# Optimization experiments

Hardware: AMD Instinct MI355X
Metric: run time of the kernel (lower is better)

Reference implementation:

```python
import jax, jax.numpy as jnp
import numpy as np

N = 100000   # nodes
E = 1600000  # edges
IN = 3       # in_channels
H = 32       # hidden_channels
C = 10       # num_classes_dynamic (== num output classes here)
G = 64       # number of graphs in the batch


def setup_inputs() -> dict:
    key = jax.random.key(0)
    ks = jax.random.split(key, 12)
    def w(k, shape, fan_in):
        return jax.random.normal(k, shape, jnp.float32) / np.sqrt(fan_in).astype(np.float32)
    inp = {}
    inp["x"] = jax.random.normal(ks[0], (N, IN), jnp.float32)
    inp["edge_index"] = jax.random.randint(ks[1], (2, E), 0, N, jnp.int32)
    inp["batch"] = jnp.sort(jax.random.randint(ks[2], (N,), 0, G, jnp.int32))
    # per-class linear filters (DynamicEdgeConv.filters)
    inp["filt_W"] = w(ks[3], (C, IN, H), IN)
    inp["filt_b"] = jnp.zeros((C, H), jnp.float32)
    # shared edge MLP: Linear(2H,H) -> ReLU -> Linear(H,H)
    inp["mlp_W1"] = w(ks[4], (2 * H, H), 2 * H)
    inp["mlp_b1"] = jnp.zeros((H,), jnp.float32)
    inp["mlp_W2"] = w(ks[5], (H, H), H)
    inp["mlp_b2"] = jnp.zeros((H,), jnp.float32)
    # GCN layers (gcn1 input dim hardcoded 323 = IN + C*H)
    inp["gcn1_W"] = w(ks[6], (IN + C * H, H), IN + C * H)
    inp["gcn1_b"] = jnp.zeros((H,), jnp.float32)
    inp["gcn2_W"] = w(ks[7], (H, H), H)
    inp["gcn2_b"] = jnp.zeros((H,), jnp.float32)
    # classifier
    inp["cls_W"] = w(ks[8], (H, C), H)
    inp["cls_b"] = jnp.zeros((C,), jnp.float32)
    return inp


def _gcn_conv(x, W, b, row, col, dinv):
    # PyG GCNConv: add self-loops, sym-normalize, aggregate src->dst
    xw = x @ W                                   # [N, H]
    norm = dinv[row] * dinv[col]                 # [E]
    out = jax.ops.segment_sum(xw[row] * norm[:, None], col, num_segments=x.shape[0])
    out = out + xw * (dinv * dinv)[:, None]      # self-loop term, norm = 1/deg_i
    return out + b


def _forward(x, edge_index, batch, filt_W, filt_b, mlp_W1, mlp_b1, mlp_W2, mlp_b2,
             gcn1_W, gcn1_b, gcn2_W, gcn2_b, cls_W, cls_b):
    row, col = edge_index[0], edge_index[1]
    n = x.shape[0]

    # DynamicEdgeConv: per-class filter -> gather(row,col) -> edge MLP -> scatter_add into col
    def per_class(_, wb):
        Wc, bc = wb
        xc = x @ Wc + bc                                      # [N, H]
        ef = jnp.concatenate([xc[row], xc[col]], axis=1)      # [E, 2H]
        h = jax.nn.relu(ef @ mlp_W1 + mlp_b1) @ mlp_W2 + mlp_b2
        return None, jax.ops.segment_sum(h, col, num_segments=n)
    _, aggs = jax.lax.scan(per_class, None, (filt_W, filt_b))  # [C, N, H]

    feat = jnp.concatenate([x, aggs.transpose(1, 0, 2).reshape(n, -1)], axis=1)  # [N, IN + C*H]

    deg = jax.ops.segment_sum(jnp.ones(row.shape[0], x.dtype), col, num_segments=n) + 1.0
    dinv = deg ** -0.5
    h1 = jax.nn.relu(_gcn_conv(feat, gcn1_W, gcn1_b, row, col, dinv))
    h2 = jax.nn.relu(_gcn_conv(h1, gcn2_W, gcn2_b, row, col, dinv))

    counts = jax.ops.segment_sum(jnp.ones(n, x.dtype), batch, num_segments=G)
    pooled = jax.ops.segment_sum(h2, batch, num_segments=G) / jnp.maximum(counts, 1.0)[:, None]
    return pooled @ cls_W + cls_b                             # [G, C]


def reference(x, edge_index, batch, filt_W, filt_b, mlp_W1, mlp_b1, mlp_W2, mlp_b2,
              gcn1_W, gcn1_b, gcn2_W, gcn2_b, cls_W, cls_b):
    return _forward(x, edge_index, batch, filt_W, filt_b, mlp_W1, mlp_b1, mlp_W2, mlp_b2,
                    gcn1_W, gcn1_b, gcn2_W, gcn2_b, cls_W, cls_b)
```

## Files before the change

kernel.cpp:

```cpp
#include <hip/hip_runtime.h>

#define NN 100000
#define NE 1600000
#define HH 32
#define CC 10
#define GG 64
#define NB 391
#define PBLK 100
#define ECH 16000
#define MTOT (NB * PBLK)
#define MSB ((MTOT + 255) / 256)

typedef _Float16 half8 __attribute__((ext_vector_type(8)));
typedef _Float16 half2v __attribute__((ext_vector_type(2)));
typedef float f32x4 __attribute__((ext_vector_type(4)));

__device__ __forceinline__ half2v bch(int v) { return __builtin_bit_cast(half2v, v); }

__global__ void zero_f(float* p, int n) {
    int i = blockIdx.x * 256 + threadIdx.x;
    if (i < n) p[i] = 0.0f;
}

__global__ void precompute_small(const float* __restrict__ fW, const float* __restrict__ fb,
                                 const float* __restrict__ W1, const float* __restrict__ b1,
                                 const float* __restrict__ W2, const float* __restrict__ b2,
                                 const float* __restrict__ g1W, float* __restrict__ tab) {
    int c = blockIdx.x;
    int k = threadIdx.x >> 5;
    int j = threadIdx.x & 31;
    float m = 0.f;
    for (int mm = 0; mm < 32; ++mm)
        m += W2[k * 32 + mm] * g1W[(3 + 32 * c + mm) * 32 + j];
    tab[2240 + c * 1024 + k * 32 + j] = m;

    if (k < 3) {
        float a = 0.f, b = 0.f;
        for (int i = 0; i < 32; ++i) {
            float w = fW[c * 96 + k * 32 + i];
            a += w * W1[i * 32 + j];
            b += w * W1[(32 + i) * 32 + j];
        }
        tab[c * 96 + k * 32 + j] = a;
        tab[960 + c * 96 + k * 32 + j] = b;
    } else if (k == 3) {
        float h = b1[j];
        for (int i = 0; i < 32; ++i)
            h += fb[c * 32 + i] * (W1[i * 32 + j] + W1[(32 + i) * 32 + j]);
        tab[1920 + c * 32 + j] = h;
    } else if (k == 4 && c == 0) {
        float t = 0.f;
        for (int cc2 = 0; cc2 < CC; ++cc2)
            for (int mm = 0; mm < 32; ++mm)
                t += b2[mm] * g1W[(3 + 32 * cc2 + mm) * 32 + j];
        tab[12480 + j] = t;
    }
}

__global__ void mfrag_kernel(const float* __restrict__ tab, _Float16* __restrict__ Mfrag) {
    int gid = blockIdx.x * 256 + threadIdx.x;
    if (gid >= 1280) return;
    int set = gid >> 6, l = gid & 63;
    int kc = set >> 1, jt = set & 1;
    int j = jt * 16 + (l & 15);
    int kbase = kc * 32 + (l >> 4) * 8;
#pragma unroll
    for (int i = 0; i < 8; ++i)
        Mfrag[gid * 8 + i] = (_Float16)tab[2240 + (kbase + i) * 32 + j];
}

__global__ void bucket_hist(const int* __restrict__ ei, int* __restrict__ mat) {
    __shared__ int h[NB];
    int blk = blockIdx.x, tid = threadIdx.x;
    for (int i = tid; i < NB; i += 256) h[i] = 0;
    __syncthreads();
    int base = blk * ECH;
    for (int k = tid; k < ECH; k += 256)
        atomicAdd(&h[ei[NE + base + k] >> 8], 1);
    __syncthreads();
    for (int i = tid; i < NB; i += 256) mat[i * PBLK + blk] = h[i];
}

__global__ void scan_m1(const int* __restrict__ mat, int* __restrict__ msum) {
    __shared__ int sh[256];
    int b = blockIdx.x, t = threadIdx.x;
    int i = b * 256 + t;
    sh[t] = (i < MTOT) ? mat[i] : 0;
    __syncthreads();
    for (int off = 128; off > 0; off >>= 1) {
        if (t < off) sh[t] += sh[t + off];
        __syncthreads();
    }
    if (t == 0) msum[b] = sh[0];
}

__global__ void scan_m2(int* __restrict__ msum) {
    __shared__ int sh[256];
    int t = threadIdx.x;
    int v = (t < MSB) ? msum[t] : 0;
    sh[t] = v;
    __syncthreads();
    for (int off = 1; off < 256; off <<= 1) {
        int add = (t >= off) ? sh[t - off] : 0;
        __syncthreads();
        sh[t] += add;
        __syncthreads();
    }
    if (t < MSB) msum[t] = sh[t] - v;
}

__global__ void scan_m3(int* __restrict__ mat, const int* __restrict__ msum) {
    __shared__ int sh[256];
    int b = blockIdx.x, t = threadIdx.x;
    int i = b * 256 + t;
    int v = (i < MTOT) ? mat[i] : 0;
    sh[t] = v;
    __syncthreads();
    for (int off = 1; off < 256; off <<= 1) {
        int add = (t >= off) ? sh[t - off] : 0;
        __syncthreads();
        sh[t] += add;
        __syncthreads();
    }
    if (i < MTOT) mat[i] = sh[t] - v + msum[b];
}

__global__ void bucket_scatter(const int* __restrict__ ei, const int* __restrict__ mat,
                               unsigned int* __restrict__ part) {
    __shared__ int bas[NB];
    __shared__ int cur[NB];
    int blk = blockIdx.x, tid = threadIdx.x;
    for (int i = tid; i < NB; i += 256) { bas[i] = mat[i * PBLK + blk]; cur[i] = 0; }
    __syncthreads();
    int base = blk * ECH;
    for (int k = tid; k < ECH; k += 256) {
        int e = base + k;
        int r = ei[e];
        int c = ei[NE + e];
        int b = c >> 8;
        int local = atomicAdd(&cur[b], 1);
        part[bas[b] + local] = (unsigned)r | ((unsigned)(c & 255) << 24);
    }
}

__global__ void bucket_build(const unsigned int* __restrict__ part, const int* __restrict__ mat,
                             const float* __restrict__ x, int* __restrict__ csr_row,
                             int* __restrict__ ideg, int* __restrict__ offs,
                             float* __restrict__ dinv, float4* __restrict__ xpad,
                             uint4* __restrict__ xs) {
    __shared__ int lh[256];
    __shared__ int lex[256];
    __shared__ int cur[256];
    int b = blockIdx.x, tid = threadIdx.x;
    int ebase = mat[b * PBLK];
    int eend = (b == NB - 1) ? NE : mat[(b + 1) * PBLK];
    int m = eend - ebase;
    lh[tid] = 0;
    __syncthreads();
    for (int k = tid; k < m; k += 256) {
        unsigned v = part[ebase + k];
        atomicAdd(&lh[v >> 24], 1);
    }
    __syncthreads();
    int cnt = lh[tid];
    lex[tid] = cnt;
    __syncthreads();
    for (int off = 1; off < 256; off <<= 1) {
        int v = (tid >= off) ? lex[tid - off] : 0;
        __syncthreads();
        lex[tid] += v;
        __syncthreads();
    }
    int excl = lex[tid] - cnt;
    lex[tid] = excl;
    cur[tid] = 0;
    int n = b * 256 + tid;
    if (n < NN) {
        ideg[n] = cnt;
        offs[n] = ebase + excl;
        float di = rsqrtf((float)cnt + 1.0f);
        dinv[n] = di;
        float x0 = x[n * 3], x1 = x[n * 3 + 1], x2 = x[n * 3 + 2];
        xpad[n] = make_float4(x0, x1, x2, di);
        _Float16 hx = (_Float16)x0, hy = (_Float16)x1, hz = (_Float16)x2;
        half2v sx = {hx, hx}, sy = {hy, hy}, sz = {hz, hz};
        xs[n] = make_uint4(__builtin_bit_cast(unsigned int, sx),
                           __builtin_bit_cast(unsigned int, sy),
                           __builtin_bit_cast(unsigned int, sz), 0u);
    }
    if (b == 0 && tid == 0) offs[NN] = NE;
    __syncthreads();
    for (int k = tid; k < m; k += 256) {
        unsigned v = part[ebase + k];
        int cl = (int)(v >> 24);
        int r = (int)(v & 0x00FFFFFFu);
        int local = atomicAdd(&cur[cl], 1);
        csr_row[ebase + lex[cl] + local] = r;
    }
}

#define EC_PAIR(QQ, SRC) do { \
    half2v px_ = bch(__shfl((int)(QQ).x, (SRC), 64)); \
    half2v py_ = bch(__shfl((int)(QQ).y, (SRC), 64)); \
    half2v pz_ = bch(__shfl((int)(QQ).z, (SRC), 64)); \
    _Pragma("unroll") \
    for (int p = 0; p < 5; ++p) { \
        half2v v = va[p] + px_ * A0[p] + py_ * A1[p] + pz_ * A2[p]; \
        v = __builtin_elementwise_max(v, zero); \
        acc[p] += v; \
    } } while (0)

#define EC_FLUSH() do { \
    _Pragma("unroll") \
    for (int p = 0; p < 5; ++p) { \
        accf[2 * p]     += (float)acc[p].x; \
        accf[2 * p + 1] += (float)acc[p].y; \
        acc[p] = zero; \
    } } while (0)

#define EC_CHUNK_FROM(T0, QQ, C2) do { \
    int tfull_ = (C2) >> 1; \
    int t_ = (T0); \
    for (; t_ + 4 <= tfull_; t_ += 4) { \
        _Pragma("unroll") \
        for (int u = 0; u < 4; ++u) EC_PAIR(QQ, 2 * (t_ + u) + half); \
        EC_FLUSH(); \
    } \
    for (; t_ < tfull_; ++t_) EC_PAIR(QQ, 2 * t_ + half); \
    if ((C2) & 1) { \
        int src_ = (C2) - 1; \
        half2v px_ = bch(__shfl((int)(QQ).x, src_, 64)); \
        half2v py_ = bch(__shfl((int)(QQ).y, src_, 64)); \
        half2v pz_ = bch(__shfl((int)(QQ).z, src_, 64)); \
        if (half == 0) { \
            _Pragma("unroll") \
            for (int p = 0; p < 5; ++p) { \
                half2v v = va[p] + px_ * A0[p] + py_ * A1[p] + pz_ * A2[p]; \
                v = __builtin_elementwise_max(v, zero); \
                acc[p] += v; \
            } \
        } \
    } \
    EC_FLUSH(); } while (0)

__global__ __launch_bounds__(256, 4) void edgeconv_fused(
    const uint4* __restrict__ xs, const int* __restrict__ offs,
    const int* __restrict__ csr_row, const float* __restrict__ tab,
    _Float16* __restrict__ aggh) {
    int lane = threadIdx.x & 63;
    int j = lane & 31;
    int half = lane >> 5;

    half2v A0[5], A1[5], A2[5], B0[5], B1[5], B2[5], hb[5];
#pragma unroll
    for (int p = 0; p < 5; ++p) {
        int c0 = 2 * p, c1 = 2 * p + 1;
        A0[p] = half2v{(_Float16)tab[c0 * 96 + j],        (_Float16)tab[c1 * 96 + j]};
        A1[p] = half2v{(_Float16)tab[c0 * 96 + 32 + j],   (_Float16)tab[c1 * 96 + 32 + j]};
        A2[p] = half2v{(_Float16)tab[c0 * 96 + 64 + j],   (_Float16)tab[c1 * 96 + 64 + j]};
        B0[p] = half2v{(_Float16)tab[960 + c0 * 96 + j],      (_Float16)tab[960 + c1 * 96 + j]};
        B1[p] = half2v{(_Float16)tab[960 + c0 * 96 + 32 + j], (_Float16)tab[960 + c1 * 96 + 32 + j]};
        B2[p] = half2v{(_Float16)tab[960 + c0 * 96 + 64 + j], (_Float16)tab[960 + c1 * 96 + 64 + j]};
        hb[p] = half2v{(_Float16)tab[1920 + c0 * 32 + j], (_Float16)tab[1920 + c1 * 32 + j]};
    }
    const half2v zero = half2v{(_Float16)0.f, (_Float16)0.f};

    int wid = blockIdx.x * 4 + (threadIdx.x >> 6);
    const int ws = gridDim.x * 4;

    int n = wid;
    if (n >= NN) return;
    int e0 = offs[n];
    int e1 = offs[n + 1];
    uint4 qn = xs[n];
    int n2 = n + ws;
    int e0n = 0, e1n = 0;
    if (n2 < NN) { e0n = offs[n2]; e1n = offs[n2 + 1]; }
    uint4 q;
    {
        int ee = e0 + lane;
        int r0 = (ee < e1) ? csr_row[ee] : 0;
        q = xs[r0];
    }

    while (true) {
        int n3 = n2 + ws;
        int e0n2 = 0, e1n2 = 0;
        if (n3 < NN) { e0n2 = offs[n3]; e1n2 = offs[n3 + 1]; }
        uint4 qn2 = make_uint4(0u, 0u, 0u, 0u);
        if (n2 < NN) qn2 = xs[n2];

        bool multi = (e1 - e0) > 64;
        int pb = multi ? (e0 + 64) : e0n;
        int pe = multi ? e1 : e1n;
        int ee2 = pb + lane;
        int rn = (ee2 < pe) ? csr_row[ee2] : 0;

        half2v pxn = bch((int)qn.x), pyn = bch((int)qn.y), pzn = bch((int)qn.z);
        half2v va[5], acc[5];
        float accf[10];
#pragma unroll
        for (int p = 0; p < 5; ++p) {
            va[p] = hb[p] + pxn * B0[p] + pyn * B1[p] + pzn * B2[p];
            acc[p] = zero;
            accf[2 * p] = 0.f;
            accf[2 * p + 1] = 0.f;
        }

        int c2 = e1 - e0;
        if (c2 > 64) c2 = 64;
        int t0 = 0;
        if ((c2 >> 1) >= 4) {
#pragma unroll
            for (int u = 0; u < 4; ++u) EC_PAIR(q, 2 * u + half);
            EC_FLUSH();
            t0 = 4;
        }
        uint4 qpre = xs[rn];
        EC_CHUNK_FROM(t0, q, c2);

        if (multi) {
            int base = e0 + 64;
            uint4 qc = qpre;
            while (true) {
                int cc = e1 - base;
                if (cc > 64) cc = 64;
                int nb = base + 64;
                bool m2 = nb < e1;
                int pb2 = m2 ? nb : e0n;
                int pe2 = m2 ? e1 : e1n;
                int ee3 = pb2 + lane;
                int rn2 = (ee3 < pe2) ? csr_row[ee3] : 0;
                uint4 qp2 = xs[rn2];
                EC_CHUNK_FROM(0, qc, cc);
                qc = qp2;
                if (!m2) break;
                base = nb;
            }
            qpre = qc;
        }

#pragma unroll
        for (int c = 0; c < 10; ++c) accf[c] += __shfl_xor(accf[c], 32, 64);
        _Float16* arow = aggh + (size_t)n * 320 + j;
#pragma unroll
        for (int i = 0; i < 5; ++i) {
            int c = half * 5 + i;
            __builtin_nontemporal_store((_Float16)accf[c], arow + c * 32);
        }

        if (n2 >= NN) return;
        n = n2;
        n2 = n3;
        e0 = e0n; e1 = e1n;
        e0n = e0n2; e1n = e1n2;
        qn = qn2;
        q = qpre;
    }
}

__global__ __launch_bounds__(256) void fold_mfma(
    const _Float16* __restrict__ aggh, const _Float16* __restrict__ MfragG,
    const float4* __restrict__ xpad, const int* __restrict__ ideg,
    const float* __restrict__ tab, const float* __restrict__ g1W,
    _Float16* __restrict__ y1) {
    __shared__ _Float16 Mf[10240];
    {
        const uint4* src = (const uint4*)MfragG;
        uint4* dst = (uint4*)Mf;
        for (int i = threadIdx.x; i < 1280; i += 256) dst[i] = src[i];
    }
    __syncthreads();

    int wave = blockIdx.x * 4 + (threadIdx.x >> 6);
    int lane = threadIdx.x & 63;
    int n0 = wave * 16;
    if (n0 >= NN) return;

    int m = lane & 15, q = lane >> 4;
    int arow_n = n0 + m;
    bool rowok = arow_n < NN;
    const _Float16* arow = aggh + (size_t)arow_n * 320 + q * 8;

    const half8* mf = (const half8*)Mf;
    f32x4 acc0 = {0.f, 0.f, 0.f, 0.f};
    f32x4 acc1 = {0.f, 0.f, 0.f, 0.f};

    for (int kc = 0; kc < 10; ++kc) {
        half8 a;
        if (rowok) a = *(const half8*)(arow + kc * 32);
        else {
#pragma unroll
            for (int i = 0; i < 8; ++i) a[i] = (_Float16)0.f;
        }
        half8 b0 = mf[(kc * 2 + 0) * 64 + lane];
        half8 b1 = mf[(kc * 2 + 1) * 64 + lane];
        acc0 = __builtin_amdgcn_mfma_f32_16x16x32_f16(a, b0, acc0, 0, 0, 0);
        acc1 = __builtin_amdgcn_mfma_f32_16x16x32_f16(a, b1, acc1, 0, 0, 0);
    }

    int jcol = lane & 15;
    float t0 = tab[12480 + jcol],      t1 = tab[12480 + 16 + jcol];
    float w00 = g1W[jcol],      w01 = g1W[32 + jcol],      w02 = g1W[64 + jcol];
    float w10 = g1W[16 + jcol], w11 = g1W[48 + jcol],      w12 = g1W[80 + jcol];
#pragma unroll
    for (int r = 0; r < 4; ++r) {
        int node = n0 + q * 4 + r;
        if (node < NN) {
            float4 xn = xpad[node];
            float dg = (float)ideg[node];
            float v0 = dg * t0 + xn.x * w00 + xn.y * w01 + xn.z * w02 + acc0[r];
            float v1 = dg * t1 + xn.x * w10 + xn.y * w11 + xn.z * w12 + acc1[r];
            y1[node * 32 + jcol]      = (_Float16)(v0 * xn.w);
            y1[node * 32 + 16 + jcol] = (_Float16)(v1 * xn.w);
        }
    }
}

__global__ __launch_bounds__(256, 8) void prop1_fused(
    const int* __restrict__ offs, const int* __restrict__ csr_row,
    const unsigned int* __restrict__ y1p, const float* __restrict__ dinv,
    const float* __restrict__ g1b, const float* __restrict__ g2W,
    unsigned int* __restrict__ y2p) {
    __shared__ float g2s[1024];
    for (int i = threadIdx.x; i < 1024; i += 256) g2s[i] = g2W[i];
    __syncthreads();

    int lane = threadIdx.x & 63;
    int l = lane & 15;
    int wid = blockIdx.x * 4 + (threadIdx.x >> 6);
    int n = wid * 4 + (lane >> 4);
    if (n >= NN) return;

    int e0 = offs[n], e1 = offs[n + 1];
    float sAl = 0.f, sAh = 0.f, sBl = 0.f, sBh = 0.f;
    int e = e0;
    if (e + 7 < e1) {
        int r[8];
#pragma unroll
        for (int u = 0; u < 8; ++u) r[u] = csr_row[e + u];
        while (true) {
            half2v p[8];
#pragma unroll
            for (int u = 0; u < 8; ++u) p[u] = __builtin_bit_cast(half2v, y1p[r[u] * 16 + l]);
            int e2 = e + 8;
            bool more = (e2 + 7 < e1);
            if (more) {
#pragma unroll
                for (int u = 0; u < 8; ++u) r[u] = csr_row[e2 + u];
            }
#pragma unroll
            for (int u = 0; u < 8; u += 2) {
                sAl += (float)p[u].x;     sAh += (float)p[u].y;
                sBl += (float)p[u + 1].x; sBh += (float)p[u + 1].y;
            }
            e = e2;
            if (!more) break;
        }
    }
    if (e + 3 < e1) {
        int r[4];
#pragma unroll
        for (int u = 0; u < 4; ++u) r[u] = csr_row[e + u];
        half2v p[4];
#pragma unroll
        for (int u = 0; u < 4; ++u) p[u] = __builtin_bit_cast(half2v, y1p[r[u] * 16 + l]);
        sAl += (float)p[0].x + (float)p[2].x; sAh += (float)p[0].y + (float)p[2].y;
        sBl += (float)p[1].x + (float)p[3].x; sBh += (float)p[1].y + (float)p[3].y;
        e += 4;
    }
    if (e + 1 < e1) {
        int r0 = csr_row[e], r1 = csr_row[e + 1];
        half2v p0 = __builtin_bit_cast(half2v, y1p[r0 * 16 + l]);
        half2v p1 = __builtin_bit_cast(half2v, y1p[r1 * 16 + l]);
        sAl += (float)p0.x; sAh += (float)p0.y;
        sBl += (float)p1.x; sBh += (float)p1.y;
        e += 2;
    }
    if (e < e1) {
        int r = csr_row[e];
        half2v p = __builtin_bit_cast(half2v, y1p[r * 16 + l]);
        sAl += (float)p.x; sAh += (float)p.y;
    }
    float di = dinv[n];
    half2v pn = __builtin_bit_cast(half2v, y1p[n * 16 + l]);
    float h1l = di * (sAl + sBl + (float)pn.x);
    float h1h = di * (sAh + sBh + (float)pn.y);
    float hl = fmaxf(h1l + g1b[2 * l], 0.f);
    float hh = fmaxf(h1h + g1b[2 * l + 1], 0.f);

    float al = 0.f, ah = 0.f;
    int base = lane & 48;
#pragma unroll
    for (int m = 0; m < 16; ++m) {
        float xl = __shfl(hl, base + m, 64);
        float xh2 = __shfl(hh, base + m, 64);
        al += xl * g2s[(2 * m) * 32 + 2 * l] + xh2 * g2s[(2 * m + 1) * 32 + 2 * l];
        ah += xl * g2s[(2 * m) * 32 + 2 * l + 1] + xh2 * g2s[(2 * m + 1) * 32 + 2 * l + 1];
    }
    half2v o = {(_Float16)(al * di), (_Float16)(ah * di)};
    y2p[n * 16 + l] = __builtin_bit_cast(unsigned int, o);
}

__global__ __launch_bounds__(256, 8) void prop2_plain(
    const int* __restrict__ offs, const int* __restrict__ csr_row,
    const unsigned int* __restrict__ y2p, const float* __restrict__ dinv,
    unsigned int* __restrict__ outp) {
    int lane = threadIdx.x & 63;
    int l = lane & 15;
    int wid = blockIdx.x * 4 + (threadIdx.x >> 6);
    int n = wid * 4 + (lane >> 4);
    if (n >= NN) return;

    int e0 = offs[n], e1 = offs[n + 1];
    float sAl = 0.f, sAh = 0.f, sBl = 0.f, sBh = 0.f;
    int e = e0;
    if (e + 7 < e1) {
        int r[8];
#pragma unroll
        for (int u = 0; u < 8; ++u) r[u] = csr_row[e + u];
        while (true) {
            half2v p[8];
#pragma unroll
            for (int u = 0; u < 8; ++u) p[u] = __builtin_bit_cast(half2v, y2p[r[u] * 16 + l]);
            int e2 = e + 8;
            bool more = (e2 + 7 < e1);
            if (more) {
#pragma unroll
                for (int u = 0; u < 8; ++u) r[u] = csr_row[e2 + u];
            }
#pragma unroll
            for (int u = 0; u < 8; u += 2) {
                sAl += (float)p[u].x;     sAh += (float)p[u].y;
                sBl += (float)p[u + 1].x; sBh += (float)p[u + 1].y;
            }
            e = e2;
            if (!more) break;
        }
    }
    if (e + 3 < e1) {
        int r[4];
#pragma unroll
        for (int u = 0; u < 4; ++u) r[u] = csr_row[e + u];
        half2v p[4];
#pragma unroll
        for (int u = 0; u < 4; ++u) p[u] = __builtin_bit_cast(half2v, y2p[r[u] * 16 + l]);
        sAl += (float)p[0].x + (float)p[2].x; sAh += (float)p[0].y + (float)p[2].y;
        sBl += (float)p[1].x + (float)p[3].x; sBh += (float)p[1].y + (float)p[3].y;
        e += 4;
    }
    if (e + 1 < e1) {
        int r0 = csr_row[e], r1 = csr_row[e + 1];
        half2v p0 = __builtin_bit_cast(half2v, y2p[r0 * 16 + l]);
        half2v p1 = __builtin_bit_cast(half2v, y2p[r1 * 16 + l]);
        sAl += (float)p0.x; sAh += (float)p0.y;
        sBl += (float)p1.x; sBh += (float)p1.y;
        e += 2;
    }
    if (e < e1) {
        int r = csr_row[e];
        half2v p = __builtin_bit_cast(half2v, y2p[r * 16 + l]);
        sAl += (float)p.x; sAh += (float)p.y;
    }
    float di = dinv[n];
    half2v pn = __builtin_bit_cast(half2v, y2p[n * 16 + l]);
    half2v o = {(_Float16)(di * (sAl + sBl + (float)pn.x)),
                (_Float16)(di * (sAh + sBh + (float)pn.y))};
    outp[n * 16 + l] = __builtin_bit_cast(unsigned int, o);
}

__global__ void pool_seg(const _Float16* __restrict__ h2, const float* __restrict__ g2b,
                         const int* __restrict__ batch, float* __restrict__ pooled,
                         float* __restrict__ counts) {
    int grp = threadIdx.x >> 5, j = threadIdx.x & 31;
    int base = (blockIdx.x * 8 + grp) * 64;
    if (base >= NN) return;
    float bj = g2b[j];
    float acc = 0.f, cnt = 0.f;
    int curg = -1;
    int lim = base + 64;
    if (lim > NN) lim = NN;
    for (int n = base; n < lim; ++n) {
        int g = batch[n];
        if (g != curg) {
            if (curg >= 0) {
                atomicAdd(&pooled[curg * 32 + j], acc);
                if (j == 0) atomicAdd(&counts[curg], cnt);
            }
            curg = g; acc = 0.f; cnt = 0.f;
        }
        acc += fmaxf((float)h2[n * 32 + j] + bj, 0.f);
        cnt += 1.f;
    }
    if (curg >= 0) {
        atomicAdd(&pooled[curg * 32 + j], acc);
        if (j == 0) atomicAdd(&counts[curg], cnt);
    }
}

__global__ void final_kernel(const float* __restrict__ pooled, const float* __restrict__ counts,
                             const float* __restrict__ clsW, const float* __restrict__ clsb,
                             float* __restrict__ out) {
    int tid = threadIdx.x;
    if (tid >= GG * CC) return;
    int g = tid / CC, cc = tid % CC;
    float inv = 1.0f / fmaxf(counts[g], 1.0f);
    float s = clsb[cc];
    for (int j = 0; j < 32; ++j) s += (pooled[g * 32 + j] * inv) * clsW[j * CC + cc];
    out[g * CC + cc] = s;
}

extern "C" void kernel_launch(void* const* d_in, const int* in_sizes, int n_in,
                              void* d_out, int out_size, void* d_ws, size_t ws_size,
                              hipStream_t stream) {
    const float* x     = (const float*)d_in[0];
    const int*   ei    = (const int*)d_in[1];
    const int*   batch = (const int*)d_in[2];
    const float* fW    = (const float*)d_in[3];
    const float* fb    = (const float*)d_in[4];
    const float* W1    = (const float*)d_in[5];
    const float* b1    = (const float*)d_in[6];
    const float* W2    = (const float*)d_in[7];
    const float* b2    = (const float*)d_in[8];
    const float* g1W   = (const float*)d_in[9];
    const float* g1b   = (const float*)d_in[10];
    const float* g2W   = (const float*)d_in[11];
    const float* g2b   = (const float*)d_in[12];
    const float* clsW  = (const float*)d_in[13];
    const float* clsb  = (const float*)d_in[14];
    float* out = (float*)d_out;

    float4*         xpad    = (float4*)d_ws;
    uint4*          xs      = (uint4*)(xpad + NN);
    _Float16*       aggh    = (_Float16*)(xs + NN);
    unsigned int*   part    = (unsigned int*)aggh;
    int*            csr_row = (int*)(aggh + (size_t)NN * 320);
    int*            mat     = (int*)(csr_row + NE);
    int*            msum    = mat + MTOT;
    int*            ideg    = msum + 256;
    int*            offs    = ideg + NN;
    float*          dinv    = (float*)(offs + NN + 1);
    float*          tab     = dinv + NN;
    _Float16*       Mfrag   = (_Float16*)(tab + 16384);
    _Float16*       y1      = Mfrag + 10240;
    unsigned int*   y2p     = (unsigned int*)(y1 + (size_t)NN * 32);
    unsigned int*   h2p     = y2p + (size_t)NN * 16;
    float*          pooled  = (float*)(h2p + (size_t)NN * 16);
    float*          counts  = pooled + GG * 32;

    const int propBlocks = (NN + 15) / 16;
    const int foldBlocks = ((NN + 15) / 16 + 3) / 4;

    zero_f<<<(GG * 33 + 255) / 256, 256, 0, stream>>>(pooled, GG * 33);
    precompute_small<<<10, 1024, 0, stream>>>(fW, fb, W1, b1, W2, b2, g1W, tab);
    mfrag_kernel<<<5, 256, 0, stream>>>(tab, Mfrag);

    bucket_hist<<<PBLK, 256, 0, stream>>>(ei, mat);
    scan_m1<<<MSB, 256, 0, stream>>>(mat, msum);
    scan_m2<<<1, 256, 0, stream>>>(msum);
    scan_m3<<<MSB, 256, 0, stream>>>(mat, msum);
    bucket_scatter<<<PBLK, 256, 0, stream>>>(ei, mat, part);
    bucket_build<<<NB, 256, 0, stream>>>(part, mat, x, csr_row, ideg, offs, dinv, xpad, xs);

    edgeconv_fused<<<2048, 256, 0, stream>>>(xs, offs, csr_row, tab, aggh);
    fold_mfma<<<foldBlocks, 256, 0, stream>>>(aggh, Mfrag, xpad, ideg, tab, g1W, y1);

    prop1_fused<<<propBlocks, 256, 0, stream>>>(offs, csr_row, (const unsigned int*)y1,
                                                dinv, g1b, g2W, y2p);
    prop2_plain<<<propBlocks, 256, 0, stream>>>(offs, csr_row, y2p, dinv, h2p);
    pool_seg<<<(NN + 511) / 512, 256, 0, stream>>>((const _Float16*)h2p, g2b, batch,
                                                   pooled, counts);
    final_kernel<<<1, 640, 0, stream>>>(pooled, counts, clsW, clsb, out);
}
```

Measured before the change: 368.8 us.

## Fuse pooling into prop2, merge small setup kernels, interleave aggh class layout

Removes the zero_f and mfrag_kernel launches by folding pooled zeroing into scan_m2 and the Mfrag fragment build into precompute_small, with the fragment index remapped to a new class-interleaved K ordering. The edgeconv output is now written as packed half2 words so each wave stores contiguous 32-bit values instead of strided half stores. prop2 now applies bias and ReLU and accumulates directly into pooled via wave-reduced atomics when all four nodes share a graph, which removes the h2 round trip and the separate pool kernel. The cost is more global atomics than the segmented pool used, and correctness relies on the fold kernel's K indexing matching the new interleaved layout.

New measurement: 491.0 us. 1.33x slower.

```diff
diff --git a/kernel.cpp b/kernel.cpp
--- a/kernel.cpp
+++ b/kernel.cpp
@@ -17,15 +17,12 @@
 
 __device__ __forceinline__ half2v bch(int v) { return __builtin_bit_cast(half2v, v); }
 
-__global__ void zero_f(float* p, int n) {
-    int i = blockIdx.x * 256 + threadIdx.x;
-    if (i < n) p[i] = 0.0f;
-}
 
 __global__ void precompute_small(const float* __restrict__ fW, const float* __restrict__ fb,
                                  const float* __restrict__ W1, const float* __restrict__ b1,
                                  const float* __restrict__ W2, const float* __restrict__ b2,
-                                 const float* __restrict__ g1W, float* __restrict__ tab) {
+                                 const float* __restrict__ g1W, float* __restrict__ tab,
+                                 _Float16* __restrict__ Mfrag) {
     int c = blockIdx.x;
     int k = threadIdx.x >> 5;
     int j = threadIdx.x & 31;
@@ -55,18 +52,19 @@
                 t += b2[mm] * g1W[(3 + 32 * cc2 + mm) * 32 + j];
         tab[12480 + j] = t;
     }
-}
-
-__global__ void mfrag_kernel(const float* __restrict__ tab, _Float16* __restrict__ Mfrag) {
-    int gid = blockIdx.x * 256 + threadIdx.x;
-    if (gid >= 1280) return;
-    int set = gid >> 6, l = gid & 63;
-    int kc = set >> 1, jt = set & 1;
-    int j = jt * 16 + (l & 15);
-    int kbase = kc * 32 + (l >> 4) * 8;
-#pragma unroll
-    for (int i = 0; i < 8; ++i)
-        Mfrag[gid * 8 + i] = (_Float16)tab[2240 + (kbase + i) * 32 + j];
+    __syncthreads();
+    {
+        int jch = k;
+        int jcol = j;
+        float v = tab[2240 + c * 1024 + jch * 32 + jcol];
+        int knew = (c >> 1) * 64 + 2 * jch + (c & 1);
+        int kc = knew >> 5, within = knew & 31;
+        int jt = jcol >> 4;
+        int lq = within >> 3, ii = within & 7;
+        int lidx = lq * 16 + (jcol & 15);
+        int flat = ((kc * 2 + jt) * 64 + lidx) * 8 + ii;
+        Mfrag[flat] = (_Float16)v;
+    }
 }
 
 __global__ void bucket_hist(const int* __restrict__ ei, int* __restrict__ mat) {
@@ -94,7 +92,8 @@
     if (t == 0) msum[b] = sh[0];
 }
 
-__global__ void scan_m2(int* __restrict__ msum) {
+__global__ void scan_m2(int* __restrict__ msum, float* __restrict__ pooled) {
+    for (int i = threadIdx.x; i < GG * 33; i += 256) pooled[i] = 0.0f;
     __shared__ int sh[256];
     int t = threadIdx.x;
     int v = (t < MSB) ? msum[t] : 0;
@@ -342,11 +341,14 @@
 
 #pragma unroll
         for (int c = 0; c < 10; ++c) accf[c] += __shfl_xor(accf[c], 32, 64);
-        _Float16* arow = aggh + (size_t)n * 320 + j;
-#pragma unroll
-        for (int i = 0; i < 5; ++i) {
-            int c = half * 5 + i;
-            __builtin_nontemporal_store((_Float16)accf[c], arow + c * 32);
+        unsigned* arow32 = (unsigned*)(aggh + (size_t)n * 320);
+        half2v d0 = {(_Float16)accf[2 * half],     (_Float16)accf[2 * half + 1]};
+        half2v d1 = {(_Float16)accf[4 + 2 * half], (_Float16)accf[4 + 2 * half + 1]};
+        arow32[lane]      = __builtin_bit_cast(unsigned, d0);
+        arow32[64 + lane] = __builtin_bit_cast(unsigned, d1);
+        if (half == 0) {
+            half2v d2 = {(_Float16)accf[8], (_Float16)accf[9]};
+            arow32[128 + lane] = __builtin_bit_cast(unsigned, d2);
         }
 
         if (n2 >= NN) return;
@@ -502,10 +504,11 @@
     y2p[n * 16 + l] = __builtin_bit_cast(unsigned int, o);
 }
 
-__global__ __launch_bounds__(256, 8) void prop2_plain(
+__global__ __launch_bounds__(256, 8) void prop2_pool(
     const int* __restrict__ offs, const int* __restrict__ csr_row,
     const unsigned int* __restrict__ y2p, const float* __restrict__ dinv,
-    unsigned int* __restrict__ outp) {
+    const int* __restrict__ batch, const float* __restrict__ g2b,
+    float* __restrict__ pooled, float* __restrict__ counts) {
     int lane = threadIdx.x & 63;
     int l = lane & 15;
     int wid = blockIdx.x * 4 + (threadIdx.x >> 6);
@@ -564,37 +567,24 @@
     }
     float di = dinv[n];
     half2v pn = __builtin_bit_cast(half2v, y2p[n * 16 + l]);
-    half2v o = {(_Float16)(di * (sAl + sBl + (float)pn.x)),
-                (_Float16)(di * (sAh + sBh + (float)pn.y))};
-    outp[n * 16 + l] = __builtin_bit_cast(unsigned int, o);
-}
-
-__global__ void pool_seg(const _Float16* __restrict__ h2, const float* __restrict__ g2b,
-                         const int* __restrict__ batch, float* __restrict__ pooled,
-                         float* __restrict__ counts) {
-    int grp = threadIdx.x >> 5, j = threadIdx.x & 31;
-    int base = (blockIdx.x * 8 + grp) * 64;
-    if (base >= NN) return;
-    float bj = g2b[j];
-    float acc = 0.f, cnt = 0.f;
-    int curg = -1;
-    int lim = base + 64;
-    if (lim > NN) lim = NN;
-    for (int n = base; n < lim; ++n) {
-        int g = batch[n];
-        if (g != curg) {
-            if (curg >= 0) {
-                atomicAdd(&pooled[curg * 32 + j], acc);
-                if (j == 0) atomicAdd(&counts[curg], cnt);
-            }
-            curg = g; acc = 0.f; cnt = 0.f;
-        }
-        acc += fmaxf((float)h2[n * 32 + j] + bj, 0.f);
-        cnt += 1.f;
-    }
-    if (curg >= 0) {
-        atomicAdd(&pooled[curg * 32 + j], acc);
-        if (j == 0) atomicAdd(&counts[curg], cnt);
+    float vl = fmaxf(di * (sAl + sBl + (float)pn.x) + g2b[2 * l], 0.f);
+    float vh = fmaxf(di * (sAh + sBh + (float)pn.y) + g2b[2 * l + 1], 0.f);
+
+    int g = batch[n];
+    int gref = __shfl(g, l, 64);
+    bool same = __all(g == gref);
+    if (same) {
+        vl += __shfl_xor(vl, 16, 64); vl += __shfl_xor(vl, 32, 64);
+        vh += __shfl_xor(vh, 16, 64); vh += __shfl_xor(vh, 32, 64);
+        if (lane < 16) {
+            atomicAdd(&pooled[gref * 32 + 2 * l], vl);
+            atomicAdd(&pooled[gref * 32 + 2 * l + 1], vh);
+            if (l == 0) atomicAdd(&counts[gref], 4.0f);
+        }
+    } else {
+        atomicAdd(&pooled[g * 32 + 2 * l], vl);
+        atomicAdd(&pooled[g * 32 + 2 * l + 1], vh);
+        if (l == 0) atomicAdd(&counts[g], 1.0f);
     }
 }
 
@@ -651,13 +641,11 @@
     const int propBlocks = (NN + 15) / 16;
     const int foldBlocks = ((NN + 15) / 16 + 3) / 4;
 
-    zero_f<<<(GG * 33 + 255) / 256, 256, 0, stream>>>(pooled, GG * 33);
-    precompute_small<<<10, 1024, 0, stream>>>(fW, fb, W1, b1, W2, b2, g1W, tab);
-    mfrag_kernel<<<5, 256, 0, stream>>>(tab, Mfrag);
+    precompute_small<<<10, 1024, 0, stream>>>(fW, fb, W1, b1, W2, b2, g1W, tab, Mfrag);
 
     bucket_hist<<<PBLK, 256, 0, stream>>>(ei, mat);
     scan_m1<<<MSB, 256, 0, stream>>>(mat, msum);
-    scan_m2<<<1, 256, 0, stream>>>(msum);
+    scan_m2<<<1, 256, 0, stream>>>(msum, pooled);
     scan_m3<<<MSB, 256, 0, stream>>>(mat, msum);
     bucket_scatter<<<PBLK, 256, 0, stream>>>(ei, mat, part);
     bucket_build<<<NB, 256, 0, stream>>>(part, mat, x, csr_row, ideg, offs, dinv, xpad, xs);
@@ -667,8 +655,7 @@
 
     prop1_fused<<<propBlocks, 256, 0, stream>>>(offs, csr_row, (const unsigned int*)y1,
                                                 dinv, g1b, g2W, y2p);
-    prop2_plain<<<propBlocks, 256, 0, stream>>>(offs, csr_row, y2p, dinv, h2p);
-    pool_seg<<<(NN + 511) / 512, 256, 0, stream>>>((const _Float16*)h2p, g2b, batch,
-                                                   pooled, counts);
+    prop2_pool<<<propBlocks, 256, 0, stream>>>(offs, csr_row, y2p, dinv, batch, g2b,
+                                               pooled, counts);
     final_kernel<<<1, 640, 0, stream>>>(pooled, counts, clsW, clsb, out);
 }
```
